# Kernel tuning notes

Hardware: AMD Instinct MI355X
Metric: run time of the kernel (lower is better)

## Reference

```python
import jax, jax.numpy as jnp
import numpy as np

B, STEP, H, N_ENC = 256, 32, 512, 60
PD, LD, NB, NTYPE, NPLAYER = 32, 32, 6, 11, 35


def _parity_masks(S):
    # Static relation-11/12 edge masks from update_adjacency_matrix (step is a Python int).
    m11 = np.zeros((S, S), dtype=bool)
    m12 = np.zeros((S, S), dtype=bool)
    for row in range(S):
        ni = row // 2
        if row % 2 == 0:
            c = (ni + 1) * 2
            if c <= S - 1:
                (m11 if ni % 2 == 0 else m12)[row, c] = True
                (m11 if ni % 2 == 0 else m12)[c, row] = True
        else:
            c = (ni + 1) * 2 + 1
            if c <= S - 1:
                (m12 if ni % 2 == 0 else m11)[row, c] = True
                (m12 if ni % 2 == 0 else m11)[c, row] = True
    return jnp.asarray(m11), jnp.asarray(m12)


def update_adjacency(adj, step, shot_type_predict=False):
    b = adj.shape[0]
    S = step * 2
    new = jnp.zeros((b, 13, S, S), dtype=adj.dtype).at[:, :, :S - 2, :S - 2].set(adj)
    m11, m12 = _parity_masks(S)
    new = new.at[:, 11].set(jnp.where(m11, 1, new[:, 11]))
    new = new.at[:, 12].set(jnp.where(m12, 1, new[:, 12]))
    if shot_type_predict:
        idx = (step - 1) * 2 if step % 2 == 0 else (step - 1) * 2 + 1
        new = new.at[:, :, idx, :].set(0).at[:, :, :, idx].set(0)
    return new


def rgcn(node, adj, layer_params):
    # adj: (B,13,N,N) int; slice off relation 0 -> 12 relations. Dropout is eval-mode identity.
    adj_f = adj[:, 1:].astype(node.dtype)  # (B,12,N,N)
    x = node
    n_layers = len(layer_params)
    for i, (basis, comb, w_self) in enumerate(layer_params):
        act = jax.nn.sigmoid if i == n_layers - 1 else jax.nn.relu
        W = jnp.einsum('rb,bij->rij', comb, basis)            # (12,H,H)
        msg = jnp.einsum('brnm,bmh->brnh', adj_f, x)          # (B,12,N,H)
        x = act(jnp.einsum('brnh,rhk->bnk', msg, W) + x @ w_self.T)
    return x


def setup_inputs() -> dict:
    key = jax.random.key(0)
    ks = jax.random.split(key, 20)
    s = 0.05
    return {
        'player': jax.random.randint(ks[0], (B, 2), 0, NPLAYER, dtype=jnp.int32),
        'step': STEP,
        'encode_node_embedding': jax.random.normal(ks[1], (B, N_ENC, H), jnp.float32),
        'adjacency_matrix': jax.random.randint(ks[2], (B, 13, (STEP - 1) * 2, (STEP - 1) * 2), 0, 2, dtype=jnp.int32),
        'player_A_x': jax.random.uniform(ks[3], (B, 1), jnp.float32),
        'player_A_y': jax.random.uniform(ks[4], (B, 1), jnp.float32),
        'player_B_x': jax.random.uniform(ks[5], (B, 1), jnp.float32),
        'player_B_y': jax.random.uniform(ks[6], (B, 1), jnp.float32),
        'emb_table': jax.random.normal(ks[7], (NPLAYER, PD), jnp.float32) * s,
        'coord_W': jax.random.normal(ks[8], (LD, 2), jnp.float32) * s,
        'coord_b': jnp.zeros((LD,), jnp.float32),
        'in_W': jax.random.normal(ks[9], (H, PD + LD), jnp.float32) * s,
        'in_b': jnp.zeros((H,), jnp.float32),
        'basis0': jax.random.normal(ks[10], (NB, H, H), jnp.float32) * s,
        'comb0': jax.random.normal(ks[11], (12, NB), jnp.float32) * s,
        'self0': jax.random.normal(ks[12], (H, H), jnp.float32) * s,
        'basis1': jax.random.normal(ks[13], (NB, H, H), jnp.float32) * s,
        'comb1': jax.random.normal(ks[14], (12, NB), jnp.float32) * s,
        'self1': jax.random.normal(ks[15], (H, H), jnp.float32) * s,
        'type_W': jax.random.normal(ks[16], (NTYPE, 2 * H), jnp.float32) * s,
        'type_b': jnp.zeros((NTYPE,), jnp.float32),
    }


def reference(player, step, encode_node_embedding, adjacency_matrix,
              player_A_x, player_A_y, player_B_x, player_B_y,
              emb_table, coord_W, coord_b, in_W, in_b,
              basis0, comb0, self0, basis1, comb1, self1, type_W, type_b):
    b = player.shape[0]
    layers = [(basis0, comb0, self0), (basis1, comb1, self1)]

    coord_A = jnp.stack([player_A_x, player_A_y], axis=2)   # (B,1,2)
    coord_B = jnp.stack([player_B_x, player_B_y], axis=2)   # (B,1,2)
    coords = jnp.stack([coord_A, coord_B], axis=2).reshape(b, -1, 2)  # (B,2,2)
    loc = jax.nn.relu(coords @ coord_W.T + coord_b)          # (B,2,LD)
    pemb = emb_table[player]                                 # (B,2,PD)
    initial = jnp.concatenate([loc, pemb], axis=-1) @ in_W.T + in_b  # (B,2,H)

    # first=False branch: current coords == prev coords, so model_input == initial
    mi = jnp.concatenate([encode_node_embedding, initial], axis=1)   # (B,62,H)
    tmp = rgcn(mi, adjacency_matrix, layers)
    passed = jnp.concatenate([encode_node_embedding[:, :-2], tmp[:, -4:]], axis=1)  # (B,62,H)

    tmp_adj = update_adjacency(adjacency_matrix, step, shot_type_predict=True)  # (B,13,64,64)
    mi2 = jnp.concatenate([passed, initial], axis=1)         # (B,64,H)
    drop = (step - 1) * 2 if step % 2 == 0 else (step - 1) * 2 + 1
    keep = np.delete(np.arange(step * 2), drop)
    mi2 = mi2[:, keep]
    tmp_adj = tmp_adj[:, :, keep][:, :, :, keep]
    tmp2 = rgcn(mi2, tmp_adj, layers)                        # (B,63,H)

    pad = jnp.zeros((b, tmp2.shape[1] + 1, tmp2.shape[2]), tmp2.dtype)
    if step % 2 == 0:
        pad = pad.at[:, :-2].set(tmp2[:, :-1]).at[:, -1].set(tmp2[:, -1])
    else:
        pad = pad.at[:, :-1].set(tmp2)
    stp = jnp.concatenate([passed[:, :-2], pad[:, -4:]], axis=1)  # (B,64,H)
    if step % 2 == 0:
        black = stp[:, (step - 1) * 2 + 1]
        white = stp[:, (step - 2) * 2]
    else:
        black = stp[:, (step - 2) * 2 + 1]
        white = stp[:, (step - 1) * 2]
    logits = jnp.concatenate([black, white], axis=-1) @ type_W.T + type_b
    return logits
```

## Files before the change

kernel.cpp:

```cpp
#include <hip/hip_runtime.h>
#include <hip/hip_bf16.h>

typedef unsigned short u16;
typedef unsigned long long u64;
typedef __attribute__((ext_vector_type(4))) short short4v;
typedef __attribute__((ext_vector_type(8))) short short8;
typedef __attribute__((ext_vector_type(4))) float floatx4;

__device__ __forceinline__ u16 f2bf(float f) {
    union { float f; unsigned u; } v; v.f = f;
    unsigned r = v.u + 0x7FFF + ((v.u >> 16) & 1);
    return (u16)(r >> 16);
}

__global__ void k_wcat(const float* __restrict__ basis, const float* __restrict__ selfW,
                       u16* __restrict__ wf) {
    int bi = blockIdx.x, t = threadIdx.x;
    int kr = t >> 7;
    int nb = (t & 127) * 4;
    for (int it = 0; it < 4; ++it) {
        int k = bi * 8 + it * 2 + kr;
        float v0, v1, v2, v3;
        if (k < 3072) {
            int q = k >> 9, h = k & 511;
            const float4 bz = *(const float4*)(basis + ((size_t)(q * 512 + h)) * 512 + nb);
            v0 = bz.x; v1 = bz.y; v2 = bz.z; v3 = bz.w;
        } else {
            int kk = k - 3072;
            v0 = selfW[(size_t)(nb + 0) * 512 + kk];
            v1 = selfW[(size_t)(nb + 1) * 512 + kk];
            v2 = selfW[(size_t)(nb + 2) * 512 + kk];
            v3 = selfW[(size_t)(nb + 3) * 512 + kk];
        }
        float vv[4] = {v0, v1, v2, v3};
        for (int i = 0; i < 4; ++i) {
            int n = nb + i;
            wf[(size_t)(k >> 5) * 16384 + (n >> 4) * 512 + ((k >> 3) & 3) * 128 + (n & 15) * 8 + (k & 7)] = f2bf(vv[i]);
        }
    }
}

__global__ void k_masks(const int* __restrict__ A, u64* __restrict__ m0, u64* __restrict__ m1) {
    int bi = blockIdx.x;
    int b = bi / 12, r = bi % 12;
    const int* Ab = A + (size_t)(b * 13 + (r + 1)) * 62 * 62;
    int lane = threadIdx.x;
    u64 my0 = 0, my1 = 0;
    for (int n = 0; n < 64; ++n) {
        int raw = 0;
        if (n < 62 && lane < 62) raw = (Ab[n * 62 + lane] != 0) ? 1 : 0;
        u64 b0 = __ballot(raw != 0);
        int v1 = 0;
        if (n < 63 && lane < 63) {
            int oi = (n == 62) ? 63 : n;
            int oj = (lane == 62) ? 63 : lane;
            v1 = (oi < 62 && oj < 62) ? raw : 0;
            int lo = (oi < oj) ? oi : oj, hi = (oi < oj) ? oj : oi;
            if (hi == lo + 2) {
                int p = (lo >> 1) & 1;
                int chp = ((lo & 1) == 0) ? (p ? 12 : 11) : (p ? 11 : 12);
                if (r + 1 == chp) v1 = 1;
            }
        }
        u64 b1 = __ballot(v1 != 0);
        if (lane == n) { my0 = b0; my1 = b1; }
    }
    m0[(size_t)bi * 64 + lane] = my0;
    m1[(size_t)bi * 64 + lane] = my1;
}

#define AQ_SETSTRIDE (256UL * 6 * 4096)
__global__ void k_aqexp(const u64* __restrict__ msk, const float* __restrict__ comb0,
                        const float* __restrict__ comb1, u16* __restrict__ aq) {
    int b = blockIdx.x >> 3, sp = blockIdx.x & 7;
    int t = threadIdx.x;
    __shared__ u64 sm[12 * 64];
    __shared__ float cmb[2][12][6];
    if (t < 72) { cmb[0][t / 6][t % 6] = comb0[t]; cmb[1][t / 6][t % 6] = comb1[t]; }
    for (int i = t; i < 768; i += 256) sm[i] = msk[(size_t)b * 768 + i];
    __syncthreads();
    #pragma unroll
    for (int ii2 = 0; ii2 < 2; ++ii2) {
        int pos = (sp * 2 + ii2) * 256 + t;
        int f = pos >> 9, lane = (pos >> 3) & 63, j = pos & 7;
        int row = ((f >> 1) << 4) + (lane & 15);
        int mb  = ((f & 1) << 5) + ((lane >> 4) << 3) + j;
        float bits[12];
        #pragma unroll
        for (int r = 0; r < 12; ++r) bits[r] = (float)((sm[r * 64 + row] >> mb) & 1ull);
        #pragma unroll
        for (int s = 0; s < 2; ++s)
            #pragma unroll
            for (int q = 0; q < 6; ++q) {
                float v = 0.f;
                #pragma unroll
                for (int r = 0; r < 12; ++r) v += bits[r] * cmb[s][r][q];
                aq[(size_t)s * AQ_SETSTRIDE + ((size_t)b * 6 + q) * 4096 + pos] = f2bf(v);
            }
    }
}

__global__ void k_prep(const int* __restrict__ player,
                       const float* __restrict__ pAx, const float* __restrict__ pAy,
                       const float* __restrict__ pBx, const float* __restrict__ pBy,
                       const float* __restrict__ emb, const float* __restrict__ cW,
                       const float* __restrict__ cb, const float* __restrict__ inW,
                       const float* __restrict__ inb,
                       u16* __restrict__ mi1, u16* __restrict__ mi2) {
    int b = blockIdx.x, t = threadIdx.x;
    __shared__ float feat[2][64];
    if (t < 64) {
        int j = t >> 5, d = t & 31;
        float X = j ? pBx[b] : pAx[b];
        float Y = j ? pBy[b] : pAy[b];
        feat[j][d] = fmaxf(cW[d * 2] * X + cW[d * 2 + 1] * Y + cb[d], 0.f);
        feat[j][32 + d] = emb[player[b * 2 + j] * 32 + d];
    }
    __syncthreads();
    for (int h = t; h < 512; h += 256) {
        float a0 = inb[h], a1 = inb[h];
        const float* wrow = inW + h * 64;
        #pragma unroll
        for (int d = 0; d < 64; ++d) {
            float wv = wrow[d];
            a0 += wv * feat[0][d];
            a1 += wv * feat[1][d];
        }
        u16 v0 = f2bf(a0), v1 = f2bf(a1);
        size_t base = (size_t)b * 64 * 512;
        mi1[base + 60 * 512 + h] = v0;
        mi1[base + 61 * 512 + h] = v1;
        mi1[base + 62 * 512 + h] = 0;
        mi1[base + 63 * 512 + h] = 0;
        mi2[base + 62 * 512 + h] = v1;
        mi2[base + 63 * 512 + h] = 0;
    }
}

__global__ void k_cast(const float* __restrict__ enc, u16* __restrict__ mi1, u16* __restrict__ mi2) {
    long long e = ((long long)blockIdx.x * 256 + threadIdx.x) * 8;
    if (e >= 256LL * 60 * 512) return;
    int b = (int)(e / (60 * 512));
    int rm = (int)(e % (60 * 512));
    int n = rm / 512, h = rm % 512;
    float4 f0 = *(const float4*)(enc + e);
    float4 f1 = *(const float4*)(enc + e + 4);
    short8 pk;
    pk[0] = (short)f2bf(f0.x); pk[1] = (short)f2bf(f0.y);
    pk[2] = (short)f2bf(f0.z); pk[3] = (short)f2bf(f0.w);
    pk[4] = (short)f2bf(f1.x); pk[5] = (short)f2bf(f1.y);
    pk[6] = (short)f2bf(f1.z); pk[7] = (short)f2bf(f1.w);
    *(short8*)(mi1 + ((size_t)b * 64 + n) * 512 + h) = pk;
    if (n < 58) *(short8*)(mi2 + ((size_t)b * 64 + n) * 512 + h) = pk;
}

__global__ __launch_bounds__(512, 1)
void k_layer(const u16* __restrict__ x, const u16* __restrict__ aq,
             const u16* __restrict__ wc, u16* __restrict__ out) {
    int b = blockIdx.x;
    int t = threadIdx.x, lane = t & 63, w = t >> 6;
    int l15 = lane & 15, lq = lane >> 4;
    const int TS = 520;
    __shared__ __align__(16) u16 T[2][64 * 520];

    const u16* xb_base = x + (size_t)b * 64 * 512;
    short8 xb[8];
    #pragma unroll
    for (int nt = 0; nt < 4; ++nt)
        #pragma unroll
        for (int kh = 0; kh < 2; ++kh) {
            int h = (w * 4 + nt) * 16 + l15;
            int j0 = kh * 32 + lq * 8;
            short8 v;
            #pragma unroll
            for (int jj = 0; jj < 8; ++jj)
                v[jj] = (short)xb_base[(size_t)(j0 + jj) * 512 + h];
            xb[nt * 2 + kh] = v;
        }

    floatx4 acc[16];
    #pragma unroll
    for (int i = 0; i < 16; ++i) acc[i] = (floatx4)(0.f);

    const u16* aqb   = aq + (size_t)b * 6 * 4096 + (size_t)lane * 8;
    const u16* wbase = wc + (size_t)lane * 8;

    auto stageA = [&](int qq, u16* buf) {
        #pragma unroll
        for (int i = 0; i < 4; ++i) {
            short8 a0 = *(const short8*)(aqb + (size_t)qq * 4096 + (i * 2 + 0) * 512);
            short8 a1 = *(const short8*)(aqb + (size_t)qq * 4096 + (i * 2 + 1) * 512);
            #pragma unroll
            for (int nt = 0; nt < 4; ++nt) {
                floatx4 tz = (floatx4)(0.f);
                tz = __builtin_amdgcn_mfma_f32_16x16x32_bf16(a0, xb[nt * 2 + 0], tz, 0, 0, 0);
                tz = __builtin_amdgcn_mfma_f32_16x16x32_bf16(a1, xb[nt * 2 + 1], tz, 0, 0, 0);
                int hcol = (w * 4 + nt) * 16 + l15;
                int mrow = i * 16 + lq * 4;
                #pragma unroll
                for (int reg = 0; reg < 4; ++reg)
                    buf[(mrow + reg) * TS + hcol] = f2bf(tz[reg]);
            }
        }
    };

    stageA(0, T[0]);
    for (int ks = 0; ks < 16; ++ks) {
        short8 af[4], bf[4];
        #pragma unroll
        for (int i = 0; i < 4; ++i)
            af[i] = *(const short8*)(xb_base + (size_t)(i * 16 + l15) * 512 + ks * 32 + lq * 8);
        #pragma unroll
        for (int nt = 0; nt < 4; ++nt)
            bf[nt] = *(const short8*)(wbase + (size_t)(96 + ks) * 16384 + (size_t)(w * 4 + nt) * 512);
        #pragma unroll
        for (int i = 0; i < 4; ++i)
            #pragma unroll
            for (int nt = 0; nt < 4; ++nt)
                acc[i * 4 + nt] = __builtin_amdgcn_mfma_f32_16x16x32_bf16(af[i], bf[nt], acc[i * 4 + nt], 0, 0, 0);
    }
    __syncthreads();

    for (int q = 0; q < 6; ++q) {
        int cur = q & 1;
        if (q < 5) stageA(q + 1, T[cur ^ 1]);
        for (int ks = 0; ks < 16; ++ks) {
            short8 af[4], bf[4];
            #pragma unroll
            for (int i = 0; i < 4; ++i)
                af[i] = *(const short8*)&T[cur][(i * 16 + l15) * TS + ks * 32 + lq * 8];
            #pragma unroll
            for (int nt = 0; nt < 4; ++nt)
                bf[nt] = *(const short8*)(wbase + (size_t)(q * 16 + ks) * 16384 + (size_t)(w * 4 + nt) * 512);
            #pragma unroll
            for (int i = 0; i < 4; ++i)
                #pragma unroll
                for (int nt = 0; nt < 4; ++nt)
                    acc[i * 4 + nt] = __builtin_amdgcn_mfma_f32_16x16x32_bf16(af[i], bf[nt], acc[i * 4 + nt], 0, 0, 0);
        }
        __syncthreads();
    }

    #pragma unroll
    for (int i = 0; i < 4; ++i)
        #pragma unroll
        for (int nt = 0; nt < 4; ++nt) {
            int n = (w * 4 + nt) * 16 + l15;
            int m0 = i * 16 + lq * 4;
            #pragma unroll
            for (int reg = 0; reg < 4; ++reg)
                out[((size_t)b * 64 + m0 + reg) * 512 + n] = f2bf(fmaxf(acc[i * 4 + nt][reg], 0.f));
        }
}

__global__ __launch_bounds__(512, 1)
void k_layer_last(const u16* __restrict__ x, const u16* __restrict__ aq,
                  const u16* __restrict__ wc, int mode,
                  u16* __restrict__ o16, float* __restrict__ o32) {
    int b = blockIdx.x;
    int t = threadIdx.x, lane = t & 63, w = t >> 6;
    int l15 = lane & 15, lq = lane >> 4;
    const int TS = 520;
    __shared__ __align__(16) u16 T[2][16 * 520];

    const u16* xb_base = x + (size_t)b * 64 * 512;
    short8 xb[8];
    #pragma unroll
    for (int nt = 0; nt < 4; ++nt)
        #pragma unroll
        for (int kh = 0; kh < 2; ++kh) {
            int h = (w * 4 + nt) * 16 + l15;
            int j0 = kh * 32 + lq * 8;
            short8 v;
            #pragma unroll
            for (int jj = 0; jj < 8; ++jj)
                v[jj] = (short)xb_base[(size_t)(j0 + jj) * 512 + h];
            xb[nt * 2 + kh] = v;
        }

    floatx4 acc[4];
    #pragma unroll
    for (int i = 0; i < 4; ++i) acc[i] = (floatx4)(0.f);

    const u16* aqb   = aq + (size_t)b * 6 * 4096 + (size_t)lane * 8;
    const u16* wbase = wc + (size_t)lane * 8;

    auto stageA = [&](int qq, u16* buf) {
        short8 a0 = *(const short8*)(aqb + (size_t)qq * 4096 + 6 * 512);
        short8 a1 = *(const short8*)(aqb + (size_t)qq * 4096 + 7 * 512);
        #pragma unroll
        for (int nt = 0; nt < 4; ++nt) {
            floatx4 tz = (floatx4)(0.f);
            tz = __builtin_amdgcn_mfma_f32_16x16x32_bf16(a0, xb[nt * 2 + 0], tz, 0, 0, 0);
            tz = __builtin_amdgcn_mfma_f32_16x16x32_bf16(a1, xb[nt * 2 + 1], tz, 0, 0, 0);
            int hcol = (w * 4 + nt) * 16 + l15;
            int mrow = lq * 4;
            #pragma unroll
            for (int reg = 0; reg < 4; ++reg)
                buf[(mrow + reg) * TS + hcol] = f2bf(tz[reg]);
        }
    };

    stageA(0, T[0]);
    for (int ks = 0; ks < 16; ++ks) {
        short8 af = *(const short8*)(xb_base + (size_t)(48 + l15) * 512 + ks * 32 + lq * 8);
        #pragma unroll
        for (int nt = 0; nt < 4; ++nt) {
            short8 bf = *(const short8*)(wbase + (size_t)(96 + ks) * 16384 + (size_t)(w * 4 + nt) * 512);
            acc[nt] = __builtin_amdgcn_mfma_f32_16x16x32_bf16(af, bf, acc[nt], 0, 0, 0);
        }
    }
    __syncthreads();

    for (int q = 0; q < 6; ++q) {
        int cur = q & 1;
        if (q < 5) stageA(q + 1, T[cur ^ 1]);
        for (int ks = 0; ks < 16; ++ks) {
            short8 af = *(const short8*)&T[cur][l15 * TS + ks * 32 + lq * 8];
            #pragma unroll
            for (int nt = 0; nt < 4; ++nt) {
                short8 bf = *(const short8*)(wbase + (size_t)(q * 16 + ks) * 16384 + (size_t)(w * 4 + nt) * 512);
                acc[nt] = __builtin_amdgcn_mfma_f32_16x16x32_bf16(af, bf, acc[nt], 0, 0, 0);
            }
        }
        __syncthreads();
    }

    #pragma unroll
    for (int nt = 0; nt < 4; ++nt) {
        int n = (w * 4 + nt) * 16 + l15;
        #pragma unroll
        for (int reg = 0; reg < 4; ++reg) {
            int m = 48 + lq * 4 + reg;
            float v = acc[nt][reg];
            if (mode == 1) {
                if (m >= 58 && m <= 61)
                    o16[((size_t)b * 64 + m) * 512 + n] = f2bf(1.f / (1.f + __expf(-v)));
            } else {
                if (m == 60 || m == 62) {
                    int slot = (m == 60) ? (b * 2) : (b * 2 + 1);
                    o32[(size_t)slot * 512 + n] = 1.f / (1.f + __expf(-v));
                }
            }
        }
    }
}

__global__ void k_final(const float* __restrict__ t2, const float* __restrict__ tW,
                        const float* __restrict__ tb, float* __restrict__ outp) {
    int b = blockIdx.x, l = threadIdx.x;
    float a[11];
    #pragma unroll
    for (int j = 0; j < 11; ++j) a[j] = 0.f;
    for (int it = 0; it < 16; ++it) {
        int h = it * 64 + l;
        float c = (h < 512) ? t2[(b * 2 + 1) * 512 + h] : t2[(b * 2 + 0) * 512 + (h - 512)];
        #pragma unroll
        for (int j = 0; j < 11; ++j) a[j] += c * tW[j * 1024 + h];
    }
    #pragma unroll
    for (int j = 0; j < 11; ++j) {
        float v = a[j];
        for (int off = 32; off > 0; off >>= 1) v += __shfl_down(v, off, 64);
        if (l == 0) outp[b * 11 + j] = v + tb[j];
    }
}

extern "C" void kernel_launch(void* const* d_in, const int* in_sizes, int n_in,
                              void* d_out, int out_size, void* d_ws, size_t ws_size,
                              hipStream_t stream) {
    const int*   player = (const int*)d_in[0];
    const float* enc    = (const float*)d_in[2];
    const int*   adjm   = (const int*)d_in[3];
    const float* pAx    = (const float*)d_in[4];
    const float* pAy    = (const float*)d_in[5];
    const float* pBx    = (const float*)d_in[6];
    const float* pBy    = (const float*)d_in[7];
    const float* emb    = (const float*)d_in[8];
    const float* cW     = (const float*)d_in[9];
    const float* cb     = (const float*)d_in[10];
    const float* inW    = (const float*)d_in[11];
    const float* inb    = (const float*)d_in[12];
    const float* basis0 = (const float*)d_in[13];
    const float* comb0  = (const float*)d_in[14];
    const float* self0  = (const float*)d_in[15];
    const float* basis1 = (const float*)d_in[16];
    const float* comb1  = (const float*)d_in[17];
    const float* self1  = (const float*)d_in[18];
    const float* typeW  = (const float*)d_in[19];
    const float* typeb  = (const float*)d_in[20];

    char* ws = (char*)d_ws;
    size_t off = 0;
    auto alloc = [&](size_t bytes) -> void* {
        void* p = ws + off;
        off = (off + bytes + 255) & ~(size_t)255;
        return p;
    };
    u16* mi1   = (u16*)alloc(256UL * 64 * 512 * 2);
    u16* mi2   = (u16*)alloc(256UL * 64 * 512 * 2);
    u16* x12   = (u16*)alloc(256UL * 64 * 512 * 2);
    u16* aqbuf = (u16*)alloc(2UL * AQ_SETSTRIDE * 2);
    u16* wcat0 = (u16*)alloc(3584UL * 512 * 2);
    u16* wcat1 = (u16*)alloc(3584UL * 512 * 2);
    u64* mm0   = (u64*)alloc(256UL * 12 * 64 * 8);
    u64* mm1   = (u64*)alloc(256UL * 12 * 64 * 8);
    u16* x12b  = mi1;
    float* t2  = (float*)x12;
    u16* aq0   = aqbuf;
    u16* aq1   = aqbuf + AQ_SETSTRIDE;

    k_wcat<<<448, 256, 0, stream>>>(basis0, self0, wcat0);
    k_wcat<<<448, 256, 0, stream>>>(basis1, self1, wcat1);
    k_masks<<<3072, 64, 0, stream>>>(adjm, mm0, mm1);
    k_aqexp<<<2048, 256, 0, stream>>>(mm0, comb0, comb1, aqbuf);
    k_prep<<<256, 256, 0, stream>>>(player, pAx, pAy, pBx, pBy, emb, cW, cb, inW, inb, mi1, mi2);
    k_cast<<<3840, 256, 0, stream>>>(enc, mi1, mi2);

    k_layer<<<256, 512, 0, stream>>>(mi1, aq0, wcat0, x12);
    k_layer_last<<<256, 512, 0, stream>>>(x12, aq1, wcat1, 1, mi2, nullptr);
    k_aqexp<<<2048, 256, 0, stream>>>(mm1, comb0, comb1, aqbuf);
    k_layer<<<256, 512, 0, stream>>>(mi2, aq0, wcat0, x12b);
    k_layer_last<<<256, 512, 0, stream>>>(x12b, aq1, wcat1, 2, nullptr, t2);

    k_final<<<256, 64, 0, stream>>>(t2, typeW, typeb, (float*)d_out);
}
```

Measured before the change: 715.2 us.

## Reassociate RGCN layer to multiply X by basis first, split blocks by output half

The first layer kernel now computes U = X·W_basis per basis and then multiplies by the combined adjacency, where it used to form A·X first and then multiply by W. Each batch's work is split across two 256-thread blocks that each own half the output columns, so two blocks can run per CU. The layer writes its output in a transposed fragment layout plus a row copy for the last layer's reads. The aq expansion is split into single-set launches, and the cast/prep and wcat kernels are merged to cut launch count. In exchange, each half-block recomputes X·W over all 64 rows and there are more aq expansion launches.

Result: slower. 866.0 us (+21.1%).

```diff
diff --git a/kernel.cpp b/kernel.cpp
--- a/kernel.cpp
+++ b/kernel.cpp
@@ -13,9 +13,14 @@
     return (u16)(r >> 16);
 }
 
-__global__ void k_wcat(const float* __restrict__ basis, const float* __restrict__ selfW,
-                       u16* __restrict__ wf) {
+__global__ void k_wcat2(const float* __restrict__ b0, const float* __restrict__ s0,
+                        const float* __restrict__ b1, const float* __restrict__ s1,
+                        u16* __restrict__ wf0, u16* __restrict__ wf1) {
     int bi = blockIdx.x, t = threadIdx.x;
+    const float* basis = (bi < 448) ? b0 : b1;
+    const float* selfW = (bi < 448) ? s0 : s1;
+    u16* wf = (bi < 448) ? wf0 : wf1;
+    if (bi >= 448) bi -= 448;
     int kr = t >> 7;
     int nb = (t & 127) * 4;
     for (int it = 0; it < 4; ++it) {
@@ -69,14 +74,13 @@
     m1[(size_t)bi * 64 + lane] = my1;
 }
 
-#define AQ_SETSTRIDE (256UL * 6 * 4096)
-__global__ void k_aqexp(const u64* __restrict__ msk, const float* __restrict__ comb0,
-                        const float* __restrict__ comb1, u16* __restrict__ aq) {
+__global__ void k_aqexp1(const u64* __restrict__ msk, const float* __restrict__ comb,
+                         u16* __restrict__ aq) {
     int b = blockIdx.x >> 3, sp = blockIdx.x & 7;
     int t = threadIdx.x;
     __shared__ u64 sm[12 * 64];
-    __shared__ float cmb[2][12][6];
-    if (t < 72) { cmb[0][t / 6][t % 6] = comb0[t]; cmb[1][t / 6][t % 6] = comb1[t]; }
+    __shared__ float cmb[72];
+    if (t < 72) cmb[t] = comb[t];
     for (int i = t; i < 768; i += 256) sm[i] = msk[(size_t)b * 768 + i];
     __syncthreads();
     #pragma unroll
@@ -89,25 +93,41 @@
         #pragma unroll
         for (int r = 0; r < 12; ++r) bits[r] = (float)((sm[r * 64 + row] >> mb) & 1ull);
         #pragma unroll
-        for (int s = 0; s < 2; ++s)
-            #pragma unroll
-            for (int q = 0; q < 6; ++q) {
-                float v = 0.f;
-                #pragma unroll
-                for (int r = 0; r < 12; ++r) v += bits[r] * cmb[s][r][q];
-                aq[(size_t)s * AQ_SETSTRIDE + ((size_t)b * 6 + q) * 4096 + pos] = f2bf(v);
-            }
-    }
-}
-
-__global__ void k_prep(const int* __restrict__ player,
-                       const float* __restrict__ pAx, const float* __restrict__ pAy,
-                       const float* __restrict__ pBx, const float* __restrict__ pBy,
-                       const float* __restrict__ emb, const float* __restrict__ cW,
-                       const float* __restrict__ cb, const float* __restrict__ inW,
-                       const float* __restrict__ inb,
-                       u16* __restrict__ mi1, u16* __restrict__ mi2) {
-    int b = blockIdx.x, t = threadIdx.x;
+        for (int q = 0; q < 6; ++q) {
+            float v = 0.f;
+            #pragma unroll
+            for (int r = 0; r < 12; ++r) v += bits[r] * cmb[r * 6 + q];
+            aq[((size_t)b * 6 + q) * 4096 + pos] = f2bf(v);
+        }
+    }
+}
+
+__global__ void k_castprep(const float* __restrict__ enc,
+                           const int* __restrict__ player,
+                           const float* __restrict__ pAx, const float* __restrict__ pAy,
+                           const float* __restrict__ pBx, const float* __restrict__ pBy,
+                           const float* __restrict__ emb, const float* __restrict__ cW,
+                           const float* __restrict__ cb, const float* __restrict__ inW,
+                           const float* __restrict__ inb,
+                           u16* __restrict__ mi1, u16* __restrict__ mi2) {
+    int t = threadIdx.x;
+    if (blockIdx.x < 3840) {
+        long long e = ((long long)blockIdx.x * 256 + t) * 8;
+        int b = (int)(e / (60 * 512));
+        int rm = (int)(e % (60 * 512));
+        int n = rm / 512, h = rm % 512;
+        float4 f0 = *(const float4*)(enc + e);
+        float4 f1 = *(const float4*)(enc + e + 4);
+        short8 pk;
+        pk[0] = (short)f2bf(f0.x); pk[1] = (short)f2bf(f0.y);
+        pk[2] = (short)f2bf(f0.z); pk[3] = (short)f2bf(f0.w);
+        pk[4] = (short)f2bf(f1.x); pk[5] = (short)f2bf(f1.y);
+        pk[6] = (short)f2bf(f1.z); pk[7] = (short)f2bf(f1.w);
+        *(short8*)(mi1 + ((size_t)b * 64 + n) * 512 + h) = pk;
+        if (n < 58) *(short8*)(mi2 + ((size_t)b * 64 + n) * 512 + h) = pk;
+        return;
+    }
+    int b = blockIdx.x - 3840;
     __shared__ float feat[2][64];
     if (t < 64) {
         int j = t >> 5, d = t & 31;
@@ -137,106 +157,86 @@
     }
 }
 
-__global__ void k_cast(const float* __restrict__ enc, u16* __restrict__ mi1, u16* __restrict__ mi2) {
-    long long e = ((long long)blockIdx.x * 256 + threadIdx.x) * 8;
-    if (e >= 256LL * 60 * 512) return;
-    int b = (int)(e / (60 * 512));
-    int rm = (int)(e % (60 * 512));
-    int n = rm / 512, h = rm % 512;
-    float4 f0 = *(const float4*)(enc + e);
-    float4 f1 = *(const float4*)(enc + e + 4);
-    short8 pk;
-    pk[0] = (short)f2bf(f0.x); pk[1] = (short)f2bf(f0.y);
-    pk[2] = (short)f2bf(f0.z); pk[3] = (short)f2bf(f0.w);
-    pk[4] = (short)f2bf(f1.x); pk[5] = (short)f2bf(f1.y);
-    pk[6] = (short)f2bf(f1.z); pk[7] = (short)f2bf(f1.w);
-    *(short8*)(mi1 + ((size_t)b * 64 + n) * 512 + h) = pk;
-    if (n < 58) *(short8*)(mi2 + ((size_t)b * 64 + n) * 512 + h) = pk;
-}
-
-__global__ __launch_bounds__(512, 1)
+__global__ __launch_bounds__(256, 2)
 void k_layer(const u16* __restrict__ x, const u16* __restrict__ aq,
-             const u16* __restrict__ wc, u16* __restrict__ out) {
-    int b = blockIdx.x;
+             const u16* __restrict__ wc, u16* __restrict__ outT, u16* __restrict__ outR) {
+    int b = blockIdx.x >> 1, nh = blockIdx.x & 1;
     int t = threadIdx.x, lane = t & 63, w = t >> 6;
     int l15 = lane & 15, lq = lane >> 4;
-    const int TS = 520;
-    __shared__ __align__(16) u16 T[2][64 * 520];
-
-    const u16* xb_base = x + (size_t)b * 64 * 512;
-    short8 xb[8];
-    #pragma unroll
-    for (int nt = 0; nt < 4; ++nt)
-        #pragma unroll
-        for (int kh = 0; kh < 2; ++kh) {
-            int h = (w * 4 + nt) * 16 + l15;
-            int j0 = kh * 32 + lq * 8;
-            short8 v;
-            #pragma unroll
-            for (int jj = 0; jj < 8; ++jj)
-                v[jj] = (short)xb_base[(size_t)(j0 + jj) * 512 + h];
-            xb[nt * 2 + kh] = v;
-        }
-
-    floatx4 acc[16];
-    #pragma unroll
-    for (int i = 0; i < 16; ++i) acc[i] = (floatx4)(0.f);
-
+    __shared__ __align__(16) u16 U[2][16384];
+
+    const u16* xrow  = x + (size_t)b * 64 * 512;
     const u16* aqb   = aq + (size_t)b * 6 * 4096 + (size_t)lane * 8;
     const u16* wbase = wc + (size_t)lane * 8;
-
-    auto stageA = [&](int qq, u16* buf) {
-        #pragma unroll
-        for (int i = 0; i < 4; ++i) {
-            short8 a0 = *(const short8*)(aqb + (size_t)qq * 4096 + (i * 2 + 0) * 512);
-            short8 a1 = *(const short8*)(aqb + (size_t)qq * 4096 + (i * 2 + 1) * 512);
-            #pragma unroll
-            for (int nt = 0; nt < 4; ++nt) {
-                floatx4 tz = (floatx4)(0.f);
-                tz = __builtin_amdgcn_mfma_f32_16x16x32_bf16(a0, xb[nt * 2 + 0], tz, 0, 0, 0);
-                tz = __builtin_amdgcn_mfma_f32_16x16x32_bf16(a1, xb[nt * 2 + 1], tz, 0, 0, 0);
-                int hcol = (w * 4 + nt) * 16 + l15;
-                int mrow = i * 16 + lq * 4;
-                #pragma unroll
-                for (int reg = 0; reg < 4; ++reg)
-                    buf[(mrow + reg) * TS + hcol] = f2bf(tz[reg]);
-            }
-        }
-    };
-
-    stageA(0, T[0]);
-    for (int ks = 0; ks < 16; ++ks) {
-        short8 af[4], bf[4];
-        #pragma unroll
-        for (int i = 0; i < 4; ++i)
-            af[i] = *(const short8*)(xb_base + (size_t)(i * 16 + l15) * 512 + ks * 32 + lq * 8);
-        #pragma unroll
-        for (int nt = 0; nt < 4; ++nt)
-            bf[nt] = *(const short8*)(wbase + (size_t)(96 + ks) * 16384 + (size_t)(w * 4 + nt) * 512);
-        #pragma unroll
-        for (int i = 0; i < 4; ++i)
-            #pragma unroll
-            for (int nt = 0; nt < 4; ++nt)
-                acc[i * 4 + nt] = __builtin_amdgcn_mfma_f32_16x16x32_bf16(af[i], bf[nt], acc[i * 4 + nt], 0, 0, 0);
-    }
-    __syncthreads();
-
-    for (int q = 0; q < 6; ++q) {
-        int cur = q & 1;
-        if (q < 5) stageA(q + 1, T[cur ^ 1]);
+    int cfb = nh * 16 + w * 4;
+
+    floatx4 accy[16];
+    #pragma unroll
+    for (int i = 0; i < 16; ++i) accy[i] = (floatx4)(0.f);
+
+    auto computeU = [&](int qq, int buf) {
+        floatx4 au[16];
+        #pragma unroll
+        for (int i = 0; i < 16; ++i) au[i] = (floatx4)(0.f);
         for (int ks = 0; ks < 16; ++ks) {
             short8 af[4], bf[4];
             #pragma unroll
             for (int i = 0; i < 4; ++i)
-                af[i] = *(const short8*)&T[cur][(i * 16 + l15) * TS + ks * 32 + lq * 8];
+                af[i] = *(const short8*)(xrow + (size_t)(i * 16 + l15) * 512 + ks * 32 + lq * 8);
             #pragma unroll
             for (int nt = 0; nt < 4; ++nt)
-                bf[nt] = *(const short8*)(wbase + (size_t)(q * 16 + ks) * 16384 + (size_t)(w * 4 + nt) * 512);
+                bf[nt] = *(const short8*)(wbase + (size_t)(qq * 16 + ks) * 16384 + (size_t)(cfb + nt) * 512);
             #pragma unroll
             for (int i = 0; i < 4; ++i)
                 #pragma unroll
                 for (int nt = 0; nt < 4; ++nt)
-                    acc[i * 4 + nt] = __builtin_amdgcn_mfma_f32_16x16x32_bf16(af[i], bf[nt], acc[i * 4 + nt], 0, 0, 0);
+                    au[i * 4 + nt] = __builtin_amdgcn_mfma_f32_16x16x32_bf16(af[i], bf[nt], au[i * 4 + nt], 0, 0, 0);
+        }
+        #pragma unroll
+        for (int i = 0; i < 4; ++i)
+            #pragma unroll
+            for (int nt = 0; nt < 4; ++nt) {
+                short4v pk;
+                #pragma unroll
+                for (int reg = 0; reg < 4; ++reg) pk[reg] = (short)f2bf(au[i * 4 + nt][reg]);
+                int a = (i >> 1) * 8192 + (w * 4 + nt) * 512 + ((i & 1) * 2 + (lq >> 1)) * 128 + l15 * 8 + (lq & 1) * 4;
+                *(short4v*)&U[buf][a] = pk;
+            }
+    };
+
+    computeU(0, 0);
+    for (int ks = 0; ks < 16; ++ks) {
+        short8 af[4], bf[4];
+        #pragma unroll
+        for (int i = 0; i < 4; ++i)
+            af[i] = *(const short8*)(xrow + (size_t)(i * 16 + l15) * 512 + ks * 32 + lq * 8);
+        #pragma unroll
+        for (int nt = 0; nt < 4; ++nt)
+            bf[nt] = *(const short8*)(wbase + (size_t)(96 + ks) * 16384 + (size_t)(cfb + nt) * 512);
+        #pragma unroll
+        for (int i = 0; i < 4; ++i)
+            #pragma unroll
+            for (int nt = 0; nt < 4; ++nt)
+                accy[i * 4 + nt] = __builtin_amdgcn_mfma_f32_16x16x32_bf16(af[i], bf[nt], accy[i * 4 + nt], 0, 0, 0);
+    }
+    __syncthreads();
+
+    for (int q = 0; q < 6; ++q) {
+        if (q < 5) computeU(q + 1, (q + 1) & 1);
+        #pragma unroll
+        for (int kk = 0; kk < 2; ++kk) {
+            short8 a_[4], ub[4];
+            #pragma unroll
+            for (int i = 0; i < 4; ++i)
+                a_[i] = *(const short8*)(aqb + (size_t)q * 4096 + (i * 2 + kk) * 512);
+            #pragma unroll
+            for (int nt = 0; nt < 4; ++nt)
+                ub[nt] = *(const short8*)&U[q & 1][kk * 8192 + (w * 4 + nt) * 512 + lane * 8];
+            #pragma unroll
+            for (int i = 0; i < 4; ++i)
+                #pragma unroll
+                for (int nt = 0; nt < 4; ++nt)
+                    accy[i * 4 + nt] = __builtin_amdgcn_mfma_f32_16x16x32_bf16(a_[i], ub[nt], accy[i * 4 + nt], 0, 0, 0);
         }
         __syncthreads();
     }
@@ -245,81 +245,80 @@
     for (int i = 0; i < 4; ++i)
         #pragma unroll
         for (int nt = 0; nt < 4; ++nt) {
-            int n = (w * 4 + nt) * 16 + l15;
-            int m0 = i * 16 + lq * 4;
-            #pragma unroll
-            for (int reg = 0; reg < 4; ++reg)
-                out[((size_t)b * 64 + m0 + reg) * 512 + n] = f2bf(fmaxf(acc[i * 4 + nt][reg], 0.f));
-        }
-}
-
-__global__ __launch_bounds__(512, 1)
-void k_layer_last(const u16* __restrict__ x, const u16* __restrict__ aq,
-                  const u16* __restrict__ wc, int mode,
-                  u16* __restrict__ o16, float* __restrict__ o32) {
-    int b = blockIdx.x;
+            short4v pk;
+            #pragma unroll
+            for (int reg = 0; reg < 4; ++reg) pk[reg] = (short)f2bf(fmaxf(accy[i * 4 + nt][reg], 0.f));
+            size_t a = (size_t)b * 32768 + (i >> 1) * 16384 + (size_t)(nh * 16 + w * 4 + nt) * 512
+                     + ((i & 1) * 2 + (lq >> 1)) * 128 + l15 * 8 + (lq & 1) * 4;
+            *(short4v*)(outT + a) = pk;
+            if (i == 3) {
+                int n = nh * 256 + w * 64 + nt * 16 + l15;
+                #pragma unroll
+                for (int reg = 0; reg < 4; ++reg)
+                    outR[((size_t)b * 16 + lq * 4 + reg) * 512 + n] = (u16)pk[reg];
+            }
+        }
+}
+
+__global__ __launch_bounds__(256, 2)
+void k_klast(const u16* __restrict__ xT, const u16* __restrict__ xr,
+             const u16* __restrict__ aq, const u16* __restrict__ wc, int mode,
+             u16* __restrict__ o16, float* __restrict__ o32) {
+    int b = blockIdx.x >> 1, nh = blockIdx.x & 1;
     int t = threadIdx.x, lane = t & 63, w = t >> 6;
     int l15 = lane & 15, lq = lane >> 4;
     const int TS = 520;
     __shared__ __align__(16) u16 T[2][16 * 520];
 
-    const u16* xb_base = x + (size_t)b * 64 * 512;
-    short8 xb[8];
-    #pragma unroll
-    for (int nt = 0; nt < 4; ++nt)
-        #pragma unroll
-        for (int kh = 0; kh < 2; ++kh) {
-            int h = (w * 4 + nt) * 16 + l15;
-            int j0 = kh * 32 + lq * 8;
-            short8 v;
-            #pragma unroll
-            for (int jj = 0; jj < 8; ++jj)
-                v[jj] = (short)xb_base[(size_t)(j0 + jj) * 512 + h];
-            xb[nt * 2 + kh] = v;
-        }
-
-    floatx4 acc[4];
-    #pragma unroll
-    for (int i = 0; i < 4; ++i) acc[i] = (floatx4)(0.f);
-
+    const u16* xTb   = xT + (size_t)b * 32768;
     const u16* aqb   = aq + (size_t)b * 6 * 4096 + (size_t)lane * 8;
     const u16* wbase = wc + (size_t)lane * 8;
-
-    auto stageA = [&](int qq, u16* buf) {
+    int cfb = nh * 16 + w * 4;
+
+    short8 xb[16];
+    #pragma unroll
+    for (int nf = 0; nf < 8; ++nf)
+        #pragma unroll
+        for (int kh = 0; kh < 2; ++kh)
+            xb[nf * 2 + kh] = *(const short8*)(xTb + kh * 16384 + (size_t)(w * 8 + nf) * 512 + (size_t)lane * 8);
+
+    floatx4 acc[4];
+    #pragma unroll
+    for (int i = 0; i < 4; ++i) acc[i] = (floatx4)(0.f);
+
+    for (int ks = 0; ks < 16; ++ks) {
+        short8 af = *(const short8*)(xr + ((size_t)b * 16 + l15) * 512 + ks * 32 + lq * 8);
+        #pragma unroll
+        for (int nt = 0; nt < 4; ++nt) {
+            short8 bf = *(const short8*)(wbase + (size_t)(96 + ks) * 16384 + (size_t)(cfb + nt) * 512);
+            acc[nt] = __builtin_amdgcn_mfma_f32_16x16x32_bf16(af, bf, acc[nt], 0, 0, 0);
+        }
+    }
+
+    auto stageA = [&](int qq, int buf) {
         short8 a0 = *(const short8*)(aqb + (size_t)qq * 4096 + 6 * 512);
         short8 a1 = *(const short8*)(aqb + (size_t)qq * 4096 + 7 * 512);
         #pragma unroll
-        for (int nt = 0; nt < 4; ++nt) {
+        for (int nf = 0; nf < 8; ++nf) {
             floatx4 tz = (floatx4)(0.f);
-            tz = __builtin_amdgcn_mfma_f32_16x16x32_bf16(a0, xb[nt * 2 + 0], tz, 0, 0, 0);
-            tz = __builtin_amdgcn_mfma_f32_16x16x32_bf16(a1, xb[nt * 2 + 1], tz, 0, 0, 0);
-            int hcol = (w * 4 + nt) * 16 + l15;
-            int mrow = lq * 4;
+            tz = __builtin_amdgcn_mfma_f32_16x16x32_bf16(a0, xb[nf * 2 + 0], tz, 0, 0, 0);
+            tz = __builtin_amdgcn_mfma_f32_16x16x32_bf16(a1, xb[nf * 2 + 1], tz, 0, 0, 0);
+            int hcol = w * 128 + nf * 16 + l15;
             #pragma unroll
             for (int reg = 0; reg < 4; ++reg)
-                buf[(mrow + reg) * TS + hcol] = f2bf(tz[reg]);
+                T[buf][(lq * 4 + reg) * TS + hcol] = f2bf(tz[reg]);
         }
     };
 
-    stageA(0, T[0]);
-    for (int ks = 0; ks < 16; ++ks) {
-        short8 af = *(const short8*)(xb_base + (size_t)(48 + l15) * 512 + ks * 32 + lq * 8);
-        #pragma unroll
-        for (int nt = 0; nt < 4; ++nt) {
-            short8 bf = *(const short8*)(wbase + (size_t)(96 + ks) * 16384 + (size_t)(w * 4 + nt) * 512);
-            acc[nt] = __builtin_amdgcn_mfma_f32_16x16x32_bf16(af, bf, acc[nt], 0, 0, 0);
-        }
-    }
+    stageA(0, 0);
     __syncthreads();
-
     for (int q = 0; q < 6; ++q) {
-        int cur = q & 1;
-        if (q < 5) stageA(q + 1, T[cur ^ 1]);
+        if (q < 5) stageA(q + 1, (q + 1) & 1);
         for (int ks = 0; ks < 16; ++ks) {
-            short8 af = *(const short8*)&T[cur][l15 * TS + ks * 32 + lq * 8];
+            short8 af = *(const short8*)&T[q & 1][l15 * TS + ks * 32 + lq * 8];
             #pragma unroll
             for (int nt = 0; nt < 4; ++nt) {
-                short8 bf = *(const short8*)(wbase + (size_t)(q * 16 + ks) * 16384 + (size_t)(w * 4 + nt) * 512);
+                short8 bf = *(const short8*)(wbase + (size_t)(q * 16 + ks) * 16384 + (size_t)(cfb + nt) * 512);
                 acc[nt] = __builtin_amdgcn_mfma_f32_16x16x32_bf16(af, bf, acc[nt], 0, 0, 0);
             }
         }
@@ -328,7 +327,7 @@
 
     #pragma unroll
     for (int nt = 0; nt < 4; ++nt) {
-        int n = (w * 4 + nt) * 16 + l15;
+        int n = nh * 256 + w * 64 + nt * 16 + l15;
         #pragma unroll
         for (int reg = 0; reg < 4; ++reg) {
             int m = 48 + lq * 4 + reg;
@@ -399,29 +398,27 @@
     };
     u16* mi1   = (u16*)alloc(256UL * 64 * 512 * 2);
     u16* mi2   = (u16*)alloc(256UL * 64 * 512 * 2);
-    u16* x12   = (u16*)alloc(256UL * 64 * 512 * 2);
-    u16* aqbuf = (u16*)alloc(2UL * AQ_SETSTRIDE * 2);
+    u16* x12T  = (u16*)alloc(256UL * 32768 * 2);
+    u16* x12r  = (u16*)alloc(256UL * 16 * 512 * 2);
+    u16* aqbuf = (u16*)alloc(256UL * 6 * 4096 * 2);
     u16* wcat0 = (u16*)alloc(3584UL * 512 * 2);
     u16* wcat1 = (u16*)alloc(3584UL * 512 * 2);
     u64* mm0   = (u64*)alloc(256UL * 12 * 64 * 8);
     u64* mm1   = (u64*)alloc(256UL * 12 * 64 * 8);
-    u16* x12b  = mi1;
-    float* t2  = (float*)x12;
-    u16* aq0   = aqbuf;
-    u16* aq1   = aqbuf + AQ_SETSTRIDE;
-
-    k_wcat<<<448, 256, 0, stream>>>(basis0, self0, wcat0);
-    k_wcat<<<448, 256, 0, stream>>>(basis1, self1, wcat1);
+    float* t2  = (float*)mi1;
+
+    k_wcat2<<<896, 256, 0, stream>>>(basis0, self0, basis1, self1, wcat0, wcat1);
     k_masks<<<3072, 64, 0, stream>>>(adjm, mm0, mm1);
-    k_aqexp<<<2048, 256, 0, stream>>>(mm0, comb0, comb1, aqbuf);
-    k_prep<<<256, 256, 0, stream>>>(player, pAx, pAy, pBx, pBy, emb, cW, cb, inW, inb, mi1, mi2);
-    k_cast<<<3840, 256, 0, stream>>>(enc, mi1, mi2);
-
-    k_layer<<<256, 512, 0, stream>>>(mi1, aq0, wcat0, x12);
-    k_layer_last<<<256, 512, 0, stream>>>(x12, aq1, wcat1, 1, mi2, nullptr);
-    k_aqexp<<<2048, 256, 0, stream>>>(mm1, comb0, comb1, aqbuf);
-    k_layer<<<256, 512, 0, stream>>>(mi2, aq0, wcat0, x12b);
-    k_layer_last<<<256, 512, 0, stream>>>(x12b, aq1, wcat1, 2, nullptr, t2);
+    k_aqexp1<<<2048, 256, 0, stream>>>(mm0, comb0, aqbuf);
+    k_castprep<<<4096, 256, 0, stream>>>(enc, player, pAx, pAy, pBx, pBy, emb, cW, cb, inW, inb, mi1, mi2);
+
+    k_layer<<<512, 256, 0, stream>>>(mi1, aqbuf, wcat0, x12T, x12r);
+    k_aqexp1<<<2048, 256, 0, stream>>>(mm0, comb1, aqbuf);
+    k_klast<<<512, 256, 0, stream>>>(x12T, x12r, aqbuf, wcat1, 1, mi2, nullptr);
+    k_aqexp1<<<2048, 256, 0, stream>>>(mm1, comb0, aqbuf);
+    k_layer<<<512, 256, 0, stream>>>(mi2, aqbuf, wcat0, x12T, x12r);
+    k_aqexp1<<<2048, 256, 0, stream>>>(mm1, comb1, aqbuf);
+    k_klast<<<512, 256, 0, stream>>>(x12T, x12r, aqbuf, wcat1, 2, nullptr, t2);
 
     k_final<<<256, 64, 0, stream>>>(t2, typeW, typeb, (float*)d_out);
 }
```
